# Kernel tuning notes

Hardware: AMD Instinct MI355X
Metric: run time of the kernel (lower is better)

Reference implementation:

```python
import jax, jax.numpy as jnp
import numpy as np
from jax import lax

DIM = 192
HEADS = 6
WS = 8
SHIFT = 4
RED = max(8, DIM // 8)  # 24
HID = 4 * DIM


def _rel_index(ws):
    coords = np.stack(np.meshgrid(np.arange(ws), np.arange(ws), indexing='ij'))  # [2,ws,ws]
    flat = coords.reshape(2, -1)
    rel = (flat[:, :, None] - flat[:, None, :]).transpose(1, 2, 0)  # [T,T,2]
    rel[:, :, 0] += ws - 1
    rel[:, :, 1] += ws - 1
    rel[:, :, 0] *= 2 * ws - 1
    return rel.sum(-1)  # [T,T]


def _build_mask(h, w, ws, shift):
    img = np.zeros((h, w))
    slices = (slice(0, -ws), slice(-ws, -shift), slice(-shift, None))
    cnt = 0
    for hs in slices:
        for wcs in slices:
            img[hs, wcs] = cnt
            cnt += 1
    mw = img.reshape(h // ws, ws, w // ws, ws).transpose(0, 2, 1, 3).reshape(-1, ws * ws)
    diff = mw[:, None, :] - mw[:, :, None]  # [nW,T,T], diff[w,i,j]=mw[w,j]-mw[w,i]
    return np.where(diff != 0, -100.0, 0.0).astype(np.float32)


def _ln(x, g, b):
    m = x.mean(-1, keepdims=True)
    v = ((x - m) ** 2).mean(-1, keepdims=True)
    return (x - m) / jnp.sqrt(v + 1e-5) * g + b


def _conv(x, k, b, pad):
    y = lax.conv_general_dilated(x, k, (1, 1), [(pad, pad), (pad, pad)],
                                 dimension_numbers=('NCHW', 'OIHW', 'NCHW'))
    return y + b[None, :, None, None]


def setup_inputs() -> dict:
    key = jax.random.key(0)
    ks = jax.random.split(key, 16)
    rn = lambda k, s, sc=0.02: jax.random.normal(k, s, dtype=jnp.float32) * sc
    C = DIM
    return {
        'x': jax.random.normal(ks[0], (4, 256 * 256, C), dtype=jnp.float32),
        'ln1_g': jnp.ones((C,), jnp.float32), 'ln1_b': jnp.zeros((C,), jnp.float32),
        'w_qkv': rn(ks[1], (3 * C, C)), 'b_qkv': jnp.zeros((3 * C,), jnp.float32),
        'rel_table': rn(ks[2], ((2 * WS - 1) ** 2, HEADS)),
        'w_proj': rn(ks[3], (C, C)), 'b_proj': jnp.zeros((C,), jnp.float32),
        'ln2_g': jnp.ones((C,), jnp.float32), 'ln2_b': jnp.zeros((C,), jnp.float32),
        'w_fc1': rn(ks[4], (HID, C)), 'b_fc1': jnp.zeros((HID,), jnp.float32),
        'w_fc2': rn(ks[5], (C, HID)), 'b_fc2': jnp.zeros((C,), jnp.float32),
        'conv1_w': rn(ks[6], (RED, C, 1, 1)), 'conv1_b': jnp.zeros((RED,), jnp.float32),
        'conv2_w': rn(ks[7], (RED, RED, 3, 3)), 'conv2_b': jnp.zeros((RED,), jnp.float32),
        'conv3_w': rn(ks[8], (C, RED, 1, 1)), 'conv3_b': jnp.zeros((C,), jnp.float32),
        'se_w1': rn(ks[9], (RED, C)), 'se_w2': rn(ks[10], (C, RED)),
        'h': 256, 'w': 256,
    }


def reference(x, ln1_g, ln1_b, w_qkv, b_qkv, rel_table, w_proj, b_proj,
              ln2_g, ln2_b, w_fc1, b_fc1, w_fc2, b_fc2,
              conv1_w, conv1_b, conv2_w, conv2_b, conv3_w, conv3_b,
              se_w1, se_w2, h, w):
    B, _, C = x.shape
    ws, T, nh = WS, WS * WS, HEADS
    hd = C // nh
    scale = hd ** -0.5

    nx = _ln(x, ln1_g, ln1_b).reshape(B, h, w, C)
    local = nx.transpose(0, 3, 1, 2)  # NCHW for LCE

    # shifted window attention
    sh = jnp.roll(nx, (-SHIFT, -SHIFT), axis=(1, 2))
    win = sh.reshape(B, h // ws, ws, w // ws, ws, C).transpose(0, 1, 3, 2, 4, 5).reshape(-1, T, C)
    qkv = (win @ w_qkv.T + b_qkv).reshape(-1, T, 3, nh, hd).transpose(2, 0, 3, 1, 4)
    q, k, v = qkv[0] * scale, qkv[1], qkv[2]  # [BW, nh, T, hd]
    attn = jnp.einsum('whid,whjd->whij', q, k)  # [BW, nh, T, T]
    bias = rel_table[_rel_index(ws).reshape(-1)].reshape(T, T, nh).transpose(2, 0, 1)
    attn = attn + bias[None]
    mask = jnp.asarray(_build_mask(h, w, ws, SHIFT))  # [nW, T, T]
    nW = mask.shape[0]
    attn = attn.reshape(B, nW, nh, T, T) + mask[None, :, None]
    attn = jax.nn.softmax(attn, axis=-1).reshape(-1, nh, T, T)
    out = jnp.einsum('whij,whjd->whid', attn, v).transpose(0, 2, 1, 3).reshape(-1, T, C)
    out = out @ w_proj.T + b_proj
    out = out.reshape(B, h // ws, w // ws, ws, ws, C).transpose(0, 1, 3, 2, 4, 5).reshape(B, h, w, C)
    out = jnp.roll(out, (SHIFT, SHIFT), axis=(1, 2))

    x1 = x + out.reshape(B, h * w, C)
    n2 = _ln(x1, ln2_g, ln2_b)
    mlp = jax.nn.gelu(n2 @ w_fc1.T + b_fc1, approximate=False) @ w_fc2.T + b_fc2
    x2 = x1 + mlp

    # LocalContextExtractor (SE-style)
    y = _conv(local, conv1_w, conv1_b, 0)
    y = _conv(y, conv2_w, conv2_b, 1)
    y = _conv(y, conv3_w, conv3_b, 0)
    y = jnp.where(y >= 0, y, 0.2 * y)  # LeakyReLU(0.2)
    pooled = y.mean(axis=(2, 3))  # [B, C]
    wgt = jax.nn.sigmoid(jax.nn.relu(pooled @ se_w1.T) @ se_w2.T)
    y = y * wgt[:, :, None, None]
    lc = y.reshape(B, C, h * w).transpose(0, 2, 1)
    return x2 + lc
```

## Files before the change

kernel.cpp:

```cpp
#include <hip/hip_runtime.h>
#include <hip/hip_bf16.h>

typedef unsigned short u16;
typedef unsigned long long u64;
typedef __attribute__((ext_vector_type(8))) short short8x;
typedef __attribute__((ext_vector_type(4))) float f32x4;
typedef __bf16 bf16x8 __attribute__((ext_vector_type(8)));

#define SCALE 0.17677669529663687f

__device__ __forceinline__ u16 f2bf(float f) {
  unsigned u = __builtin_bit_cast(unsigned, f);
  unsigned r = (u + 0x7FFFu + ((u >> 16) & 1u)) >> 16;
  return (u16)r;
}
__device__ __forceinline__ float bf2f(u16 h) {
  return __builtin_bit_cast(float, ((unsigned)h) << 16);
}
__device__ __forceinline__ float gelu_f(float v) {
  float t = v * v;
  float a = __builtin_fmaf(t, -0.07135481627f, -1.59576912161f);
  float e = __expf(v * a);
  return v * __builtin_amdgcn_rcpf(1.0f + e);
}
__device__ __forceinline__ int swz(int row, int col, int ld) {
  return row * ld + ((((col >> 3) ^ (row & 7)) << 3) | (col & 7));
}
__device__ __forceinline__ short8x ldfrag(const u16* s, int row, int kb, int ld) {
  return *(const short8x*)(s + row * ld + (((kb >> 3) ^ (row & 7)) << 3));
}
__device__ __forceinline__ short8x ldg8(const u16* p) { return *(const short8x*)p; }

__device__ __forceinline__ f32x4 MFMA(short8x a, short8x b, f32x4 c) {
  return __builtin_amdgcn_mfma_f32_16x16x32_bf16(
      __builtin_bit_cast(bf16x8, a), __builtin_bit_cast(bf16x8, b), c, 0, 0, 0);
}
__device__ __forceinline__ u64 pack4(float a, float b, float c, float d) {
  return (u64)f2bf(a) | ((u64)f2bf(b) << 16) | ((u64)f2bf(c) << 32) | ((u64)f2bf(d) << 48);
}

__global__ void cvt_kernel(const float* __restrict__ wqkv, const float* __restrict__ wproj,
                           const float* __restrict__ wfc1, const float* __restrict__ wfc2,
                           const float* __restrict__ c1, const float* __restrict__ c3,
                           const float* __restrict__ c2,
                           u16* oq, u16* op, u16* o1, u16* o2, u16* oc1, u16* oc3,
                           float* ow2r) {
  int i = blockIdx.x * 256 + threadIdx.x;
  if (i < 110592) { float f = wqkv[i]; if (i < 36864) f *= SCALE; oq[i] = f2bf(f); return; }
  i -= 110592;
  if (i < 36864) { op[i] = f2bf(wproj[i]); return; }
  i -= 36864;
  if (i < 147456) { o1[i] = f2bf(wfc1[i]); return; }
  i -= 147456;
  if (i < 147456) { o2[i] = f2bf(wfc2[i]); return; }
  i -= 147456;
  if (i < 6144) { int r = i / 192, c = i - r * 192; oc1[i] = (r < 24) ? f2bf(c1[r * 192 + c]) : (u16)0; return; }
  i -= 6144;
  if (i < 6144) { int cc = i >> 5, k = i & 31; oc3[i] = (k < 24) ? f2bf(c3[cc * 24 + k]) : (u16)0; return; }
  i -= 6144;
  if (i < 5184) { int t = i / 576, rr = i - t * 576; int ci = rr / 24, co = rr - ci * 24;
                  ow2r[i] = c2[co * 216 + ci * 9 + t]; }
}

__global__ __launch_bounds__(256) void ln1_kernel(const float* __restrict__ x,
                                                  const float* __restrict__ g,
                                                  const float* __restrict__ b,
                                                  u16* __restrict__ nx) {
  const int wid = threadIdx.x >> 6, lane = threadIdx.x & 63;
  const int row = blockIdx.x * 4 + wid;
  const float* xr = x + row * 192;
  f32x4 v = {0.f, 0.f, 0.f, 0.f};
  if (lane < 48) v = *(const f32x4*)(xr + lane * 4);
  float s = v[0] + v[1] + v[2] + v[3];
  for (int m = 1; m < 64; m <<= 1) s += __shfl_xor(s, m);
  const float mean = s * (1.0f / 192.0f);
  f32x4 d;
#pragma unroll
  for (int r = 0; r < 4; ++r) d[r] = v[r] - mean;
  float q = (lane < 48) ? (d[0] * d[0] + d[1] * d[1] + d[2] * d[2] + d[3] * d[3]) : 0.f;
  for (int m = 1; m < 64; m <<= 1) q += __shfl_xor(q, m);
  const float rstd = rsqrtf(q * (1.0f / 192.0f) + 1e-5f);
  if (lane < 48) {
    const f32x4 gg = *(const f32x4*)(g + lane * 4);
    const f32x4 bb = *(const f32x4*)(b + lane * 4);
    u64 pk = pack4(d[0] * rstd * gg[0] + bb[0], d[1] * rstd * gg[1] + bb[1],
                   d[2] * rstd * gg[2] + bb[2], d[3] * rstd * gg[3] + bb[3]);
    *(u64*)(nx + row * 192 + lane * 4) = pk;
  }
}

__global__ __launch_bounds__(512, 4) void attn_kernel(
    const u16* __restrict__ nx, const u16* __restrict__ wq,
    const float* __restrict__ bqkv, const float* __restrict__ rel,
    u16* __restrict__ vT, u16* __restrict__ aout) {
  __shared__ u16 sQK[64 * 384];
  __shared__ float sRel[1350];
  __shared__ int sG[64];

  const int tid = threadIdx.x, blk = blockIdx.x;
  const int b = blk >> 10, wi = (blk >> 5) & 31, wj = blk & 31;
  const int wv = tid >> 6, lane = tid & 63, lr = lane & 15, hi = lane >> 4;
  u16* vTw = vT + blk * 12288;

  for (int i = tid; i < 1350; i += 512) sRel[i] = rel[i];
  if (tid < 64) {
    int si = (wi * 8 + (tid >> 3) + 4) & 255, sj = (wj * 8 + (tid & 7) + 4) & 255;
    sG[tid] = b * 65536 + si * 256 + sj;
  }
  for (int i = tid; i < 64 * 96; i += 512) {
    int r = i / 96, w32 = i - r * 96;
    int si = (wi * 8 + (r >> 3) + 4) & 255, sj = (wj * 8 + (r & 7) + 4) & 255;
    int grow = b * 65536 + si * 256 + sj;
    unsigned v = ((const unsigned*)nx)[grow * 96 + w32];
    ((unsigned*)sQK)[r * 192 + ((((w32 >> 2) ^ (r & 7)) << 2) | (w32 & 3))] = v;
  }
  __syncthreads();

  f32x4 acc[4][4] = {};
  if (wv < 6) {
    const int wbase = wv * 64;
#pragma unroll
    for (int kk = 0; kk < 6; ++kk) {
      short8x Xf[4];
#pragma unroll
      for (int tt = 0; tt < 4; ++tt) Xf[tt] = ldfrag(sQK, tt * 16 + lr, kk * 32 + hi * 8, 384);
#pragma unroll
      for (int wt = 0; wt < 4; ++wt) {
        short8x Wf = ldg8(wq + (wbase + wt * 16 + lr) * 192 + kk * 32 + hi * 8);
#pragma unroll
        for (int tt = 0; tt < 4; ++tt) acc[wt][tt] = MFMA(Wf, Xf[tt], acc[wt][tt]);
      }
    }
  } else {
    const int vbase = (wv - 6) * 96;
#pragma unroll
    for (int half = 0; half < 2; ++half) {
      short8x Bf[3][6];
      float bv[3];
#pragma unroll
      for (int j = 0; j < 3; ++j) {
        const int vc = vbase + (half * 3 + j) * 16 + lr;
#pragma unroll
        for (int kk = 0; kk < 6; ++kk)
          Bf[j][kk] = ldg8(wq + (384 + vc) * 192 + kk * 32 + hi * 8);
        bv[j] = bqkv[384 + vc];
      }
#pragma unroll
      for (int mt = 0; mt < 4; ++mt) {
        f32x4 vacc[3] = {};
#pragma unroll
        for (int kk = 0; kk < 6; ++kk) {
          short8x A = ldfrag(sQK, mt * 16 + lr, kk * 32 + hi * 8, 384);
#pragma unroll
          for (int j = 0; j < 3; ++j) vacc[j] = MFMA(A, Bf[j][kk], vacc[j]);
        }
#pragma unroll
        for (int j = 0; j < 3; ++j) {
          u64 pk = pack4(vacc[j][0] + bv[j], vacc[j][1] + bv[j],
                         vacc[j][2] + bv[j], vacc[j][3] + bv[j]);
          *(u64*)(vTw + (vbase + (half * 3 + j) * 16 + lr) * 64 + mt * 16 + hi * 4) = pk;
        }
      }
    }
  }
  __syncthreads();

  if (wv < 6) {
    const int wbase = wv * 64;
#pragma unroll
    for (int wt = 0; wt < 4; ++wt) {
      const int oc0 = wbase + wt * 16 + hi * 4;
      const f32x4 bq = *(const f32x4*)(bqkv + oc0);
      const float sc = (oc0 < 192) ? SCALE : 1.0f;
#pragma unroll
      for (int tt = 0; tt < 4; ++tt) {
        u64 pk = pack4(acc[wt][tt][0] + bq[0] * sc, acc[wt][tt][1] + bq[1] * sc,
                       acc[wt][tt][2] + bq[2] * sc, acc[wt][tt][3] + bq[3] * sc);
        *(u64*)&sQK[swz(tt * 16 + lr, oc0, 384)] = pk;
      }
    }
  }
  __syncthreads();

  f32x4 S[3][4];
#pragma unroll
  for (int i = 0; i < 3; ++i) {
    const int s = wv + 8 * i, h3 = s >> 2, q = s & 3;
    short8x Aq = ldfrag(sQK, q * 16 + lr, h3 * 32 + hi * 8, 384);
#pragma unroll
    for (int nt = 0; nt < 4; ++nt) {
      short8x Bk = ldfrag(sQK, nt * 16 + lr, 192 + h3 * 32 + hi * 8, 384);
      S[i][nt] = MFMA(Aq, Bk, (f32x4){0.f, 0.f, 0.f, 0.f});
    }
#pragma unroll
    for (int r = 0; r < 4; ++r) {
      const int tI = q * 16 + hi * 4 + r;
      const int tri = tI >> 3, trj = tI & 7;
      const int ui = wi * 8 + tri, vi = wj * 8 + trj;
      const int rgi = (ui >= 248) + (ui >= 252), cgi = (vi >= 248) + (vi >= 252);
#pragma unroll
      for (int nt = 0; nt < 4; ++nt) {
        const int tJ = nt * 16 + lr;
        const int tci = tJ >> 3, tcj = tJ & 7;
        const int idx = (tri - tci + 7) * 15 + (trj - tcj + 7);
        float v = S[i][nt][r] + sRel[idx * 6 + h3];
        const int uj = wi * 8 + tci, vj = wj * 8 + tcj;
        const int rgj = (uj >= 248) + (uj >= 252), cgj = (vj >= 248) + (vj >= 252);
        if ((rgi != rgj) | (cgi != cgj)) v -= 100.0f;
        S[i][nt][r] = v;
      }
    }
#pragma unroll
    for (int r = 0; r < 4; ++r) {
      float mx = fmaxf(fmaxf(S[i][0][r], S[i][1][r]), fmaxf(S[i][2][r], S[i][3][r]));
      mx = fmaxf(mx, __shfl_xor(mx, 1));
      mx = fmaxf(mx, __shfl_xor(mx, 2));
      mx = fmaxf(mx, __shfl_xor(mx, 4));
      mx = fmaxf(mx, __shfl_xor(mx, 8));
      float sm = 0.f;
#pragma unroll
      for (int nt = 0; nt < 4; ++nt) { float e = __expf(S[i][nt][r] - mx); S[i][nt][r] = e; sm += e; }
      sm += __shfl_xor(sm, 1); sm += __shfl_xor(sm, 2);
      sm += __shfl_xor(sm, 4); sm += __shfl_xor(sm, 8);
      const float inv = 1.0f / sm;
#pragma unroll
      for (int nt = 0; nt < 4; ++nt) S[i][nt][r] *= inv;
    }
  }
  __syncthreads();

#pragma unroll
  for (int i = 0; i < 3; ++i) {
    const int s = wv + 8 * i, h3 = s >> 2, q = s & 3;
#pragma unroll
    for (int r = 0; r < 4; ++r)
#pragma unroll
      for (int nt = 0; nt < 4; ++nt)
        sQK[h3 * 4096 + swz(q * 16 + hi * 4 + r, nt * 16 + lr, 64)] = f2bf(S[i][nt][r]);
  }
  __syncthreads();

#pragma unroll
  for (int i = 0; i < 3; ++i) {
    const int t = wv + 8 * i, h3 = t >> 2, dt = (t >> 1) & 1, tth = t & 1;
    f32x4 oacc[2] = {};
#pragma unroll
    for (int kk = 0; kk < 2; ++kk) {
      short8x Va = ldg8(vTw + (h3 * 32 + dt * 16 + lr) * 64 + kk * 32 + hi * 8);
#pragma unroll
      for (int t2 = 0; t2 < 2; ++t2) {
        short8x Pf = ldfrag(sQK + h3 * 4096, tth * 32 + t2 * 16 + lr, kk * 32 + hi * 8, 64);
        oacc[t2] = MFMA(Va, Pf, oacc[t2]);
      }
    }
#pragma unroll
    for (int t2 = 0; t2 < 2; ++t2) {
      const int token = tth * 32 + t2 * 16 + lr;
      const int grow = sG[token];
      u64 pk = pack4(oacc[t2][0], oacc[t2][1], oacc[t2][2], oacc[t2][3]);
      *(u64*)(aout + grow * 192 + h3 * 32 + dt * 16 + hi * 4) = pk;
    }
  }
}

__global__ __launch_bounds__(256) void conv1_kernel(const u16* __restrict__ nx,
                                                    const u16* __restrict__ w1,
                                                    const float* __restrict__ b1,
                                                    float* __restrict__ y1) {
  const int tid = threadIdx.x, wv = tid >> 6, lane = tid & 63, lr = lane & 15, hi = lane >> 4;
  const int g0 = blockIdx.x * 64;
  const int mt = wv;
  short8x Af[6];
#pragma unroll
  for (int kk = 0; kk < 6; ++kk)
    Af[kk] = ldg8(nx + (g0 + mt * 16 + lr) * 192 + kk * 32 + hi * 8);
  const int bI = g0 >> 16;
  const int hw0 = g0 & 65535;
#pragma unroll
  for (int nt = 0; nt < 2; ++nt) {
    f32x4 acc = {0.f, 0.f, 0.f, 0.f};
#pragma unroll
    for (int kk = 0; kk < 6; ++kk) {
      short8x Bf = ldg8(w1 + (nt * 16 + lr) * 192 + kk * 32 + hi * 8);
      acc = MFMA(Af[kk], Bf, acc);
    }
    const int c = nt * 16 + lr;
    if (c < 24) {
      const float bb = b1[c];
#pragma unroll
      for (int r = 0; r < 4; ++r) {
        const int pix = hw0 + mt * 16 + hi * 4 + r;
        y1[(bI * 24 + c) * 65536 + pix] = acc[r] + bb;
      }
    }
  }
}

__global__ __launch_bounds__(256) void conv2_kernel(const float* __restrict__ y1,
                                                    const float* __restrict__ w2r,
                                                    const float* __restrict__ cb2,
                                                    u16* __restrict__ y2) {
  const int j = threadIdx.x;
  const int i = blockIdx.x & 255;
  const int b = blockIdx.x >> 8;
  float acc[24];
#pragma unroll
  for (int r = 0; r < 24; ++r) acc[r] = cb2[r];
  const float* base = y1 + b * 24 * 65536;
  for (int t = 0; t < 9; ++t) {
    const int dh = t / 3 - 1, dw = t % 3 - 1;
    const int ii = i + dh, jj = j + dw;
    const bool ok = (ii >= 0) & (ii < 256) & (jj >= 0) & (jj < 256);
    const int offc = ok ? (ii * 256 + jj) : 0;
    const float* wt = w2r + t * 576;
    float v[24];
#pragma unroll
    for (int ci = 0; ci < 24; ++ci) {
      float vv = base[ci * 65536 + offc];
      v[ci] = ok ? vv : 0.0f;
    }
#pragma unroll
    for (int ci = 0; ci < 24; ++ci)
#pragma unroll
      for (int co = 0; co < 24; ++co)
        acc[co] += v[ci] * wt[ci * 24 + co];
  }
  u16* o = y2 + (b * 65536 + i * 256 + j) * 32;
#pragma unroll
  for (int r = 0; r < 24; ++r) o[r] = f2bf(acc[r]);
  ((unsigned long long*)(o + 24))[0] = 0ull;
  ((unsigned long long*)(o + 24))[1] = 0ull;
}

__global__ __launch_bounds__(256) void conv3_kernel(const u16* __restrict__ y2,
                                                    const u16* __restrict__ w3,
                                                    const float* __restrict__ b3,
                                                    u16* __restrict__ y,
                                                    float* __restrict__ pooled) {
  const int tid = threadIdx.x, wv = tid >> 6, lane = tid & 63, lr = lane & 15, hi = lane >> 4;
  const int g0 = blockIdx.x * 64;
  short8x Af[4];
#pragma unroll
  for (int mt = 0; mt < 4; ++mt)
    Af[mt] = ldg8(y2 + (g0 + mt * 16 + lr) * 32 + hi * 8);
  const int bI = g0 >> 16;
#pragma unroll
  for (int nt0 = 0; nt0 < 3; ++nt0) {
    const int c = (wv * 3 + nt0) * 16 + lr;
    short8x Bf = ldg8(w3 + c * 32 + hi * 8);
    const float bb = b3[c];
    float colsum = 0.f;
#pragma unroll
    for (int mt = 0; mt < 4; ++mt) {
      f32x4 acc = {0.f, 0.f, 0.f, 0.f};
      acc = MFMA(Af[mt], Bf, acc);
#pragma unroll
      for (int r = 0; r < 4; ++r) {
        float v = acc[r] + bb;
        v = (v >= 0.f) ? v : 0.2f * v;
        y[(g0 + mt * 16 + hi * 4 + r) * 192 + c] = f2bf(v);
        colsum += v;
      }
    }
    colsum += __shfl_xor(colsum, 16);
    colsum += __shfl_xor(colsum, 32);
    if (hi == 0) atomicAdd(&pooled[bI * 192 + c], colsum);
  }
}

__global__ void se_kernel(const float* __restrict__ pooled, const float* __restrict__ w1,
                          const float* __restrict__ w2, float* __restrict__ wgt) {
  __shared__ float t[24];
  const int b = blockIdx.x, lane = threadIdx.x;
  if (lane < 24) {
    float s = 0.f;
    for (int c = 0; c < 192; ++c) s += pooled[b * 192 + c] * (1.0f / 65536.0f) * w1[lane * 192 + c];
    t[lane] = fmaxf(s, 0.0f);
  }
  __syncthreads();
  for (int c = lane; c < 192; c += 64) {
    float s = 0.f;
#pragma unroll
    for (int r = 0; r < 24; ++r) s += t[r] * w2[c * 24 + r];
    wgt[b * 192 + c] = 1.0f / (1.0f + __expf(-s));
  }
}

__global__ __launch_bounds__(768, 6) void pmlp_kernel(
    const float* __restrict__ x, const u16* __restrict__ aout,
    const u16* __restrict__ wp, const float* __restrict__ bproj,
    const float* __restrict__ g2, const float* __restrict__ b2,
    const u16* __restrict__ w1m, const float* __restrict__ bf1,
    const u16* __restrict__ w2m, const float* __restrict__ bf2,
    const u16* __restrict__ y, const float* __restrict__ wgt, float* __restrict__ out) {
  __shared__ u16 sN[64 * 192];
  __shared__ u16 sH[64 * 192];
  const int tid = threadIdx.x, wv = tid >> 6, lane = tid & 63, lr = lane & 15, hi = lane >> 4;
  const int g0 = blockIdx.x * 64;
  const int ocol = wv * 16 + lr;

  f32x4 x1v[4];
  {
    f32x4 pacc[4] = {};
#pragma unroll
    for (int kk = 0; kk < 6; ++kk) {
      short8x Wf = ldg8(wp + ocol * 192 + kk * 32 + hi * 8);
#pragma unroll
      for (int mt = 0; mt < 4; ++mt)
        pacc[mt] = MFMA(ldg8(aout + (g0 + mt * 16 + lr) * 192 + kk * 32 + hi * 8), Wf, pacc[mt]);
    }
    const float bb = bproj[ocol];
#pragma unroll
    for (int mt = 0; mt < 4; ++mt)
#pragma unroll
      for (int r = 0; r < 4; ++r) {
        x1v[mt][r] = x[(g0 + mt * 16 + hi * 4 + r) * 192 + ocol] + pacc[mt][r] + bb;
        sN[swz(mt * 16 + hi * 4 + r, ocol, 192)] = f2bf(x1v[mt][r]);
      }
  }
  __syncthreads();

  for (int row = wv; row < 64; row += 12) {
    float v0 = bf2f(sN[swz(row, lane, 192)]);
    float v1 = bf2f(sN[swz(row, lane + 64, 192)]);
    float v2 = bf2f(sN[swz(row, lane + 128, 192)]);
    float s = v0 + v1 + v2;
    for (int m = 1; m < 64; m <<= 1) s += __shfl_xor(s, m);
    const float mean = s * (1.0f / 192.0f);
    const float d0 = v0 - mean, d1 = v1 - mean, d2 = v2 - mean;
    float q = d0 * d0 + d1 * d1 + d2 * d2;
    for (int m = 1; m < 64; m <<= 1) q += __shfl_xor(q, m);
    const float rstd = rsqrtf(q * (1.0f / 192.0f) + 1e-5f);
    sN[swz(row, lane, 192)]       = f2bf(d0 * rstd * g2[lane] + b2[lane]);
    sN[swz(row, lane + 64, 192)]  = f2bf(d1 * rstd * g2[lane + 64] + b2[lane + 64]);
    sN[swz(row, lane + 128, 192)] = f2bf(d2 * rstd * g2[lane + 128] + b2[lane + 128]);
  }
  __syncthreads();

  f32x4 acc[4] = {};
  for (int c = 0; c < 4; ++c) {
    const int hcol = c * 192 + wv * 16 + lr;
    f32x4 a1[4] = {};
#pragma unroll
    for (int kk = 0; kk < 6; ++kk) {
      short8x B = ldg8(w1m + hcol * 192 + kk * 32 + hi * 8);
#pragma unroll
      for (int mt = 0; mt < 4; ++mt)
        a1[mt] = MFMA(ldfrag(sN, mt * 16 + lr, kk * 32 + hi * 8, 192), B, a1[mt]);
    }
    if (c) __syncthreads();
    const float bb1 = bf1[hcol];
#pragma unroll
    for (int mt = 0; mt < 4; ++mt)
#pragma unroll
      for (int r = 0; r < 4; ++r)
        sH[swz(mt * 16 + hi * 4 + r, wv * 16 + lr, 192)] = f2bf(gelu_f(a1[mt][r] + bb1));
    __syncthreads();
#pragma unroll
    for (int kk = 0; kk < 6; ++kk) {
      short8x B = ldg8(w2m + (wv * 16 + lr) * 768 + c * 192 + kk * 32 + hi * 8);
#pragma unroll
      for (int mt = 0; mt < 4; ++mt)
        acc[mt] = MFMA(ldfrag(sH, mt * 16 + lr, kk * 32 + hi * 8, 192), B, acc[mt]);
    }
  }

  const int bI = g0 >> 16;
  const float bb = bf2[ocol];
  const float wg = wgt[bI * 192 + ocol];
#pragma unroll
  for (int mt = 0; mt < 4; ++mt)
#pragma unroll
    for (int r = 0; r < 4; ++r) {
      const int grow = g0 + mt * 16 + hi * 4 + r;
      const float lc = bf2f(y[grow * 192 + ocol]) * wg;
      out[grow * 192 + ocol] = x1v[mt][r] + acc[mt][r] + bb + lc;
    }
}

extern "C" void kernel_launch(void* const* d_in, const int* in_sizes, int n_in,
                              void* d_out, int out_size, void* d_ws, size_t ws_size,
                              hipStream_t stream) {
  const float* x     = (const float*)d_in[0];
  const float* ln1g  = (const float*)d_in[1];
  const float* ln1b  = (const float*)d_in[2];
  const float* wqkv  = (const float*)d_in[3];
  const float* bqkv  = (const float*)d_in[4];
  const float* rel   = (const float*)d_in[5];
  const float* wproj = (const float*)d_in[6];
  const float* bproj = (const float*)d_in[7];
  const float* ln2g  = (const float*)d_in[8];
  const float* ln2b  = (const float*)d_in[9];
  const float* wfc1  = (const float*)d_in[10];
  const float* bfc1  = (const float*)d_in[11];
  const float* wfc2  = (const float*)d_in[12];
  const float* bfc2  = (const float*)d_in[13];
  const float* c1w   = (const float*)d_in[14];
  const float* c1b   = (const float*)d_in[15];
  const float* c2w   = (const float*)d_in[16];
  const float* c2b   = (const float*)d_in[17];
  const float* c3w   = (const float*)d_in[18];
  const float* c3b   = (const float*)d_in[19];
  const float* sew1  = (const float*)d_in[20];
  const float* sew2  = (const float*)d_in[21];

  char* ws = (char*)d_ws;
  u16*   nx   = (u16*)(ws + 0);
  float* y1   = (float*)(ws + 100663296);
  u16*   y2   = (u16*)(ws + 125829120);
  u16*   yb   = (u16*)(ws + 142606336);
  u16*   wq   = (u16*)(ws + 243269632);
  u16*   wp   = (u16*)(ws + 243490816);
  u16*   w1m  = (u16*)(ws + 243564544);
  u16*   w2m  = (u16*)(ws + 243859456);
  u16*   cw1  = (u16*)(ws + 244154368);
  u16*   cw3  = (u16*)(ws + 244166656);
  float* w2r  = (float*)(ws + 244178944);
  float* pool = (float*)(ws + 244199680);
  float* wgt  = (float*)(ws + 244202752);
  float* out  = (float*)d_out;
  u16*   vT   = yb;
  u16*   aout = nx;

  hipMemsetAsync(pool, 0, 3072, stream);
  cvt_kernel<<<1797, 256, 0, stream>>>(wqkv, wproj, wfc1, wfc2, c1w, c3w, c2w,
                                       wq, wp, w1m, w2m, cw1, cw3, w2r);
  ln1_kernel<<<65536, 256, 0, stream>>>(x, ln1g, ln1b, nx);
  conv1_kernel<<<4096, 256, 0, stream>>>(nx, cw1, c1b, y1);
  attn_kernel<<<4096, 512, 0, stream>>>(nx, wq, bqkv, rel, vT, aout);
  conv2_kernel<<<1024, 256, 0, stream>>>(y1, w2r, c2b, y2);
  conv3_kernel<<<4096, 256, 0, stream>>>(y2, cw3, c3b, yb, pool);
  se_kernel<<<4, 64, 0, stream>>>(pool, sew1, sew2, wgt);
  pmlp_kernel<<<4096, 768, 0, stream>>>(x, aout, wp, bproj, ln2g, ln2b,
                                        w1m, bfc1, w2m, bfc2, yb, wgt, out);
}
```

Baseline: 1.160 ms.

## Transpose MFMA operands in fused proj+MLP kernel for vectorized epilogues and 2x2 tiling

Swaps the MFMA operand order so each lane holds four consecutive output channels, which turns the epilogue into packed 64-bit bf16 stores and 128-bit float loads and stores instead of scalar accesses. The MLP phase now gives each wave a 32-token by 32-channel tile instead of 64 by 16, so each global weight fragment feeds two MFMAs and each shared-memory activation fragment is reused across two weight tiles. The residual x1 is no longer kept in registers: it is written back as bf16 into the attention-output buffer and reread in the final epilogue. That lowers register pressure but gives the residual bf16 precision and adds a global round trip.

Measured after the change: 1.294 ms. +11.6%, slower.

```diff
diff --git a/kernel.cpp b/kernel.cpp
--- a/kernel.cpp
+++ b/kernel.cpp
@@ -387,7 +387,7 @@
 }
 
 __global__ __launch_bounds__(768, 6) void pmlp_kernel(
-    const float* __restrict__ x, const u16* __restrict__ aout,
+    const float* __restrict__ x, u16* __restrict__ aout,
     const u16* __restrict__ wp, const float* __restrict__ bproj,
     const float* __restrict__ g2, const float* __restrict__ b2,
     const u16* __restrict__ w1m, const float* __restrict__ bf1,
@@ -397,26 +397,30 @@
   __shared__ u16 sH[64 * 192];
   const int tid = threadIdx.x, wv = tid >> 6, lane = tid & 63, lr = lane & 15, hi = lane >> 4;
   const int g0 = blockIdx.x * 64;
-  const int ocol = wv * 16 + lr;
-
-  f32x4 x1v[4];
+
   {
     f32x4 pacc[4] = {};
 #pragma unroll
     for (int kk = 0; kk < 6; ++kk) {
-      short8x Wf = ldg8(wp + ocol * 192 + kk * 32 + hi * 8);
-#pragma unroll
-      for (int mt = 0; mt < 4; ++mt)
-        pacc[mt] = MFMA(ldg8(aout + (g0 + mt * 16 + lr) * 192 + kk * 32 + hi * 8), Wf, pacc[mt]);
-    }
-    const float bb = bproj[ocol];
-#pragma unroll
-    for (int mt = 0; mt < 4; ++mt)
-#pragma unroll
-      for (int r = 0; r < 4; ++r) {
-        x1v[mt][r] = x[(g0 + mt * 16 + hi * 4 + r) * 192 + ocol] + pacc[mt][r] + bb;
-        sN[swz(mt * 16 + hi * 4 + r, ocol, 192)] = f2bf(x1v[mt][r]);
-      }
+      short8x Wf = ldg8(wp + (wv * 16 + lr) * 192 + kk * 32 + hi * 8);
+#pragma unroll
+      for (int tt = 0; tt < 4; ++tt) {
+        short8x Bt = ldg8(aout + (g0 + tt * 16 + lr) * 192 + kk * 32 + hi * 8);
+        pacc[tt] = MFMA(Wf, Bt, pacc[tt]);
+      }
+    }
+    __syncthreads();
+    const int oc0 = wv * 16 + hi * 4;
+    const f32x4 bb4 = *(const f32x4*)(bproj + oc0);
+#pragma unroll
+    for (int tt = 0; tt < 4; ++tt) {
+      const int grow = g0 + tt * 16 + lr;
+      const f32x4 xv = *(const f32x4*)(x + grow * 192 + oc0);
+      u64 pk = pack4(xv[0] + pacc[tt][0] + bb4[0], xv[1] + pacc[tt][1] + bb4[1],
+                     xv[2] + pacc[tt][2] + bb4[2], xv[3] + pacc[tt][3] + bb4[3]);
+      *(u64*)&sN[swz(tt * 16 + lr, oc0, 192)] = pk;
+      *(u64*)(aout + grow * 192 + oc0) = pk;
+    }
   }
   __syncthreads();
 
@@ -437,45 +441,68 @@
   }
   __syncthreads();
 
-  f32x4 acc[4] = {};
+  const int th = (wv >= 6) ? 1 : 0;
+  const int cs = wv - 6 * th;
+  f32x4 acc2[2][2] = {};
   for (int c = 0; c < 4; ++c) {
-    const int hcol = c * 192 + wv * 16 + lr;
-    f32x4 a1[4] = {};
+    f32x4 a1[2][2] = {};
 #pragma unroll
     for (int kk = 0; kk < 6; ++kk) {
-      short8x B = ldg8(w1m + hcol * 192 + kk * 32 + hi * 8);
-#pragma unroll
-      for (int mt = 0; mt < 4; ++mt)
-        a1[mt] = MFMA(ldfrag(sN, mt * 16 + lr, kk * 32 + hi * 8, 192), B, a1[mt]);
+      short8x B0 = ldfrag(sN, th * 32 + lr, kk * 32 + hi * 8, 192);
+      short8x B1 = ldfrag(sN, th * 32 + 16 + lr, kk * 32 + hi * 8, 192);
+#pragma unroll
+      for (int wt = 0; wt < 2; ++wt) {
+        short8x Wf = ldg8(w1m + (c * 192 + cs * 32 + wt * 16 + lr) * 192 + kk * 32 + hi * 8);
+        a1[wt][0] = MFMA(Wf, B0, a1[wt][0]);
+        a1[wt][1] = MFMA(Wf, B1, a1[wt][1]);
+      }
     }
     if (c) __syncthreads();
-    const float bb1 = bf1[hcol];
-#pragma unroll
-    for (int mt = 0; mt < 4; ++mt)
+#pragma unroll
+    for (int wt = 0; wt < 2; ++wt) {
+      const int h0 = cs * 32 + wt * 16 + hi * 4;
+      const f32x4 b1v = *(const f32x4*)(bf1 + c * 192 + h0);
+#pragma unroll
+      for (int tt = 0; tt < 2; ++tt) {
+        const int tok = th * 32 + tt * 16 + lr;
+        u64 pk = pack4(gelu_f(a1[wt][tt][0] + b1v[0]), gelu_f(a1[wt][tt][1] + b1v[1]),
+                       gelu_f(a1[wt][tt][2] + b1v[2]), gelu_f(a1[wt][tt][3] + b1v[3]));
+        *(u64*)&sH[swz(tok, h0, 192)] = pk;
+      }
+    }
+    __syncthreads();
+#pragma unroll
+    for (int kk = 0; kk < 6; ++kk) {
+      short8x H0 = ldfrag(sH, th * 32 + lr, kk * 32 + hi * 8, 192);
+      short8x H1 = ldfrag(sH, th * 32 + 16 + lr, kk * 32 + hi * 8, 192);
+#pragma unroll
+      for (int wt = 0; wt < 2; ++wt) {
+        short8x W2 = ldg8(w2m + (cs * 32 + wt * 16 + lr) * 768 + c * 192 + kk * 32 + hi * 8);
+        acc2[wt][0] = MFMA(W2, H0, acc2[wt][0]);
+        acc2[wt][1] = MFMA(W2, H1, acc2[wt][1]);
+      }
+    }
+  }
+
+  const int bI = g0 >> 16;
+#pragma unroll
+  for (int wt = 0; wt < 2; ++wt) {
+    const int oc0 = cs * 32 + wt * 16 + hi * 4;
+    const f32x4 bb = *(const f32x4*)(bf2 + oc0);
+    const f32x4 wg = *(const f32x4*)(wgt + bI * 192 + oc0);
+#pragma unroll
+    for (int tt = 0; tt < 2; ++tt) {
+      const int grow = g0 + th * 32 + tt * 16 + lr;
+      const u64 x1p = *(const u64*)(aout + grow * 192 + oc0);
+      const u64 yv = *(const u64*)(y + grow * 192 + oc0);
+      f32x4 o;
 #pragma unroll
       for (int r = 0; r < 4; ++r)
-        sH[swz(mt * 16 + hi * 4 + r, wv * 16 + lr, 192)] = f2bf(gelu_f(a1[mt][r] + bb1));
-    __syncthreads();
-#pragma unroll
-    for (int kk = 0; kk < 6; ++kk) {
-      short8x B = ldg8(w2m + (wv * 16 + lr) * 768 + c * 192 + kk * 32 + hi * 8);
-#pragma unroll
-      for (int mt = 0; mt < 4; ++mt)
-        acc[mt] = MFMA(ldfrag(sH, mt * 16 + lr, kk * 32 + hi * 8, 192), B, acc[mt]);
-    }
-  }
-
-  const int bI = g0 >> 16;
-  const float bb = bf2[ocol];
-  const float wg = wgt[bI * 192 + ocol];
-#pragma unroll
-  for (int mt = 0; mt < 4; ++mt)
-#pragma unroll
-    for (int r = 0; r < 4; ++r) {
-      const int grow = g0 + mt * 16 + hi * 4 + r;
-      const float lc = bf2f(y[grow * 192 + ocol]) * wg;
-      out[grow * 192 + ocol] = x1v[mt][r] + acc[mt][r] + bb + lc;
-    }
+        o[r] = bf2f((u16)(x1p >> (16 * r))) + acc2[wt][tt][r] + bb[r] +
+               bf2f((u16)(yv >> (16 * r))) * wg[r];
+      *(f32x4*)(out + grow * 192 + oc0) = o;
+    }
+  }
 }
 
 extern "C" void kernel_launch(void* const* d_in, const int* in_sizes, int n_in,
```
